# Kernel optimization log

Measured on AMD Instinct MI355X. Metric: run time of the kernel, lower is better.

Reference implementation:

```python
import jax, jax.numpy as jnp
import numpy as np

N_NEURONS = 256
P_MAX = 8
N_BLOCKS = P_MAX + 1
HIDDEN = 32
BATCH = 8192


def setup_inputs() -> dict:
    key = jax.random.key(0)
    ks = jax.random.split(key, 9)
    z = jax.random.normal(ks[0], (BATCH, N_BLOCKS * N_NEURONS), dtype=jnp.float32)
    # Per-block ScalarMLP params, stacked over the n_blocks axis.
    s1 = 1.0 / np.sqrt(N_NEURONS)
    s2 = 1.0 / np.sqrt(HIDDEN)
    gW1 = jax.random.uniform(ks[1], (N_BLOCKS, N_NEURONS, HIDDEN), jnp.float32, -s1, s1)
    gb1 = jax.random.uniform(ks[2], (N_BLOCKS, HIDDEN), jnp.float32, -s1, s1)
    gW2 = jax.random.uniform(ks[3], (N_BLOCKS, HIDDEN, HIDDEN), jnp.float32, -s2, s2)
    gb2 = jax.random.uniform(ks[4], (N_BLOCKS, HIDDEN), jnp.float32, -s2, s2)
    gW3 = jax.random.uniform(ks[5], (N_BLOCKS, HIDDEN), jnp.float32, -s2, s2)
    gb3 = jax.random.uniform(ks[6], (N_BLOCKS,), jnp.float32, -s2, s2)
    # Lag coupling matrices W_r ~ U(-init_scale, init_scale), init_scale=0.1
    W = jax.random.uniform(ks[7], (P_MAX, N_NEURONS, N_NEURONS), jnp.float32, -0.1, 0.1)
    return {"z": z, "gW1": gW1, "gb1": gb1, "gW2": gW2, "gb2": gb2,
            "gW3": gW3, "gb3": gb3, "W": W}


def _energy(z, gW1, gb1, gW2, gb2, gW3, gb3, W):
    B = z.shape[0]
    blocks = z.reshape(B, N_BLOCKS, N_NEURONS)           # (B, K, n)
    # Per-block ScalarMLP energies (all blocks at once).
    h1 = jax.nn.silu(jnp.einsum('bkn,knh->bkh', blocks, gW1) + gb1)   # (B, K, H)
    h2 = jax.nn.silu(jnp.einsum('bkh,khg->bkg', h1, gW2) + gb2)       # (B, K, H)
    e = jnp.einsum('bkh,kh->bk', h2, gW3) + gb3                        # (B, K)
    # Bilinear lag couplings: z_future^T W_r z_{lag-r}, r = 1..p_max.
    z_future = blocks[:, P_MAX, :]                                     # (B, n)
    lags = blocks[:, :P_MAX, :][:, ::-1, :]                            # (B, p, n), index r-1 == block p_max-r
    cross = jnp.einsum('bi,rij,brj->b', z_future, W, lags)             # (B,)
    return e.sum(axis=-1) + cross                                      # (B,)


def reference(z, gW1, gb1, gW2, gb2, gW3, gb3, W):
    # Score s(z) = -grad_z U(z); sum over batch gives per-sample grads
    # since energies are independent across samples.
    grad_z = jax.grad(lambda zz: _energy(zz, gW1, gb1, gW2, gb2, gW3, gb3, W).sum())(z)
    return -grad_z
```

## Files before the change

### kernel.cpp

```cpp
#include <hip/hip_runtime.h>
#include <hip/hip_bf16.h>
#include <math.h>

#define BATCH 8192
#define NB 9
#define NN 256
#define PMAX 8
#define HID 32
#define ZDIM 2304

typedef short bf16x8 __attribute__((ext_vector_type(8)));
typedef float f32x4 __attribute__((ext_vector_type(4)));

static __device__ inline unsigned short f2bf(float f) {
    __hip_bfloat16 h = __float2bfloat16(f);
    return *reinterpret_cast<unsigned short*>(&h);
}

static __device__ inline uint4 pack8(float4 a, float4 b) {
    uint4 u;
    u.x = (unsigned)f2bf(a.x) | ((unsigned)f2bf(a.y) << 16);
    u.y = (unsigned)f2bf(a.z) | ((unsigned)f2bf(a.w) << 16);
    u.z = (unsigned)f2bf(b.x) | ((unsigned)f2bf(b.y) << 16);
    u.w = (unsigned)f2bf(b.z) | ((unsigned)f2bf(b.w) << 16);
    return u;
}

__global__ __launch_bounds__(256) void k_pack(
    const float* __restrict__ W, const float* __restrict__ gW1,
    unsigned short* __restrict__ Wb, unsigned short* __restrict__ WTb,
    unsigned short* __restrict__ gW1b, unsigned short* __restrict__ g1Tb) {
    int r = blockIdx.z;
    int t = threadIdx.x;
    if (r < 8) {
        __shared__ float tt[32][33];
        int i0 = blockIdx.y * 32;
        int j0 = blockIdx.x * 32;
        int tx = t & 31;
        int ty = t >> 5;
        const float* src = W + (size_t)r * 65536;
        #pragma unroll
        for (int s = 0; s < 32; s += 8) {
            float v = src[(size_t)(i0 + ty + s) * 256 + (j0 + tx)];
            tt[ty + s][tx] = v;
            Wb[(size_t)r * 65536 + (size_t)(i0 + ty + s) * 256 + (j0 + tx)] = f2bf(v);
        }
        __syncthreads();
        #pragma unroll
        for (int s = 0; s < 32; s += 8)
            WTb[(size_t)r * 65536 + (size_t)(j0 + ty + s) * 256 + (i0 + tx)] = f2bf(tt[tx][ty + s]);
    } else {
        int tg = (blockIdx.y * 8 + blockIdx.x) * 256 + t;
        for (int e = tg; e < 73728; e += 16384) {
            float v = gW1[e];
            unsigned short b = f2bf(v);
            gW1b[e] = b;
            int k = e >> 13, n = (e >> 5) & 255, h = e & 31;
            g1Tb[(size_t)(k * 32 + h) * 256 + n] = b;
        }
    }
}

__global__ __launch_bounds__(256) void k_mlp(
    const float* __restrict__ z, const unsigned short* __restrict__ g1Tb,
    const float* __restrict__ gb1, const float* __restrict__ gW2,
    const float* __restrict__ gb2, const float* __restrict__ gW3,
    float* __restrict__ d1ws) {
    __shared__ uint4 As4[2][512];
    __shared__ uint4 Bw[1024];
    __shared__ uint4 W2Ts4[128];
    __shared__ uint4 W2Ns4[128];

    int t = threadIdx.x;
    int lane = t & 63;
    int w = t >> 6;
    int k = blockIdx.y;
    int b0 = blockIdx.x * 128;

    const unsigned short* bsrc = g1Tb + (size_t)k * 8192;
    for (int e = t; e < 1024; e += 256) {
        int h = e >> 5;
        int rest = e & 31;
        int c = rest >> 2, qq = rest & 3;
        Bw[c * 128 + (h & 15) + 16 * qq + 64 * (h >> 4)] =
            *(const uint4*)(bsrc + (size_t)h * 256 + c * 32 + qq * 8);
    }
    const float* gw2 = gW2 + (size_t)k * 1024;
    unsigned short* w2t = (unsigned short*)W2Ts4;
    unsigned short* w2n = (unsigned short*)W2Ns4;
    for (int e = t; e < 1024; e += 256) {
        int n = e >> 5, kk = e & 31;
        int qq = kk >> 3, jj = kk & 7;
        int ci = (n & 15) + 16 * qq + 64 * (n >> 4);
        w2t[ci * 8 + jj] = f2bf(gw2[kk * 32 + n]);
        w2n[ci * 8 + jj] = f2bf(gw2[n * 32 + kk]);
    }

    int mq = t >> 2;
    int q = t & 3;
    int ci0 = (mq & 15) + 16 * q + 64 * (mq >> 4);

    f32x4 acc1[2][2];
    #pragma unroll
    for (int i = 0; i < 2; ++i)
        #pragma unroll
        for (int j = 0; j < 2; ++j) acc1[i][j] = (f32x4){0.f, 0.f, 0.f, 0.f};

    auto loadZ = [&](int c, float4 (&fa)[2][2]) {
        #pragma unroll
        for (int pp = 0; pp < 2; ++pp) {
            int m = mq + 64 * pp;
            const float* as = z + (size_t)(b0 + m) * ZDIM + k * 256 + c * 32 + q * 8;
            fa[pp][0] = *(const float4*)(as);
            fa[pp][1] = *(const float4*)(as + 4);
        }
    };
    auto storeA = [&](int buf, float4 (&fa)[2][2]) {
        #pragma unroll
        for (int pp = 0; pp < 2; ++pp)
            As4[buf][ci0 + 256 * pp] = pack8(fa[pp][0], fa[pp][1]);
    };

    {
        float4 fa[2][2];
        loadZ(0, fa);
        storeA(0, fa);
    }
    int cur = 0;
    for (int c = 0; c < 8; ++c) {
        __syncthreads();
        float4 fan[2][2];
        if (c < 7) loadZ(c + 1, fan);
        bf16x8 af[2], bfr[2];
        #pragma unroll
        for (int i = 0; i < 2; ++i) af[i] = __builtin_bit_cast(bf16x8, As4[cur][lane + (w * 2 + i) * 64]);
        #pragma unroll
        for (int j = 0; j < 2; ++j) bfr[j] = __builtin_bit_cast(bf16x8, Bw[c * 128 + lane + j * 64]);
        #pragma unroll
        for (int i = 0; i < 2; ++i)
            #pragma unroll
            for (int j = 0; j < 2; ++j)
                acc1[i][j] = __builtin_amdgcn_mfma_f32_16x16x32_bf16(af[i], bfr[j], acc1[i][j], 0, 0, 0);
        if (c < 7) storeA(cur ^ 1, fan);
        cur ^= 1;
    }

    int cq = lane >> 4;
    int ci16 = lane & 15;
    float b1v[2], b2v[2], g3v[2];
    #pragma unroll
    for (int j = 0; j < 2; ++j) {
        b1v[j] = gb1[k * 32 + j * 16 + ci16];
        b2v[j] = gb2[k * 32 + j * 16 + ci16];
        g3v[j] = gW3[k * 32 + j * 16 + ci16];
    }
    unsigned short* Hs = (unsigned short*)As4;
    float sp1[2][2][4];
    __syncthreads();
    #pragma unroll
    for (int i = 0; i < 2; ++i)
        #pragma unroll
        for (int j = 0; j < 2; ++j)
            #pragma unroll
            for (int r = 0; r < 4; ++r) {
                float a1 = acc1[i][j][r] + b1v[j];
                float s1 = 1.f / (1.f + __expf(-a1));
                sp1[i][j][r] = s1 * (1.f + a1 * (1.f - s1));
                int row = w * 32 + i * 16 + cq * 4 + r;
                int col = j * 16 + ci16;
                int chunk = (row & 15) + 16 * (col >> 3) + 64 * (row >> 4);
                Hs[chunk * 8 + (col & 7)] = f2bf(a1 * s1);
            }
    __syncthreads();

    bf16x8 af2[2], wf[2];
    #pragma unroll
    for (int i = 0; i < 2; ++i) af2[i] = __builtin_bit_cast(bf16x8, As4[0][lane + (w * 2 + i) * 64]);
    #pragma unroll
    for (int j = 0; j < 2; ++j) wf[j] = __builtin_bit_cast(bf16x8, W2Ts4[lane + j * 64]);
    f32x4 acc2[2][2];
    #pragma unroll
    for (int i = 0; i < 2; ++i)
        #pragma unroll
        for (int j = 0; j < 2; ++j) {
            acc2[i][j] = (f32x4){0.f, 0.f, 0.f, 0.f};
            acc2[i][j] = __builtin_amdgcn_mfma_f32_16x16x32_bf16(af2[i], wf[j], acc2[i][j], 0, 0, 0);
        }

    __syncthreads();
    #pragma unroll
    for (int i = 0; i < 2; ++i)
        #pragma unroll
        for (int j = 0; j < 2; ++j)
            #pragma unroll
            for (int r = 0; r < 4; ++r) {
                float a2 = acc2[i][j][r] + b2v[j];
                float s2 = 1.f / (1.f + __expf(-a2));
                float da2 = g3v[j] * s2 * (1.f + a2 * (1.f - s2));
                int row = w * 32 + i * 16 + cq * 4 + r;
                int col = j * 16 + ci16;
                int chunk = (row & 15) + 16 * (col >> 3) + 64 * (row >> 4);
                Hs[chunk * 8 + (col & 7)] = f2bf(da2);
            }
    __syncthreads();

    bf16x8 af3[2], wg[2];
    #pragma unroll
    for (int i = 0; i < 2; ++i) af3[i] = __builtin_bit_cast(bf16x8, As4[0][lane + (w * 2 + i) * 64]);
    #pragma unroll
    for (int j = 0; j < 2; ++j) wg[j] = __builtin_bit_cast(bf16x8, W2Ns4[lane + j * 64]);
    #pragma unroll
    for (int i = 0; i < 2; ++i)
        #pragma unroll
        for (int j = 0; j < 2; ++j) {
            f32x4 a3 = (f32x4){0.f, 0.f, 0.f, 0.f};
            a3 = __builtin_amdgcn_mfma_f32_16x16x32_bf16(af3[i], wg[j], a3, 0, 0, 0);
            #pragma unroll
            for (int r = 0; r < 4; ++r) {
                int row = w * 32 + i * 16 + cq * 4 + r;
                int col = j * 16 + ci16;
                d1ws[((size_t)k * BATCH + b0 + row) * 32 + col] = a3[r] * sp1[i][j][r];
            }
        }
}

__global__ __launch_bounds__(256) void k_gemm_lo(
    const float* __restrict__ z, const float* __restrict__ d1,
    const unsigned short* __restrict__ WTb, const unsigned short* __restrict__ gW1b,
    float* __restrict__ out) {
    __shared__ uint4 As4[2][512];
    __shared__ uint4 Bs4[2][512];

    int t = threadIdx.x;
    int lane = t & 63;
    int w = t >> 6;
    int wr = w >> 1, wc = w & 1;
    int b0 = blockIdx.x * 128;
    int n0 = blockIdx.y * 128;
    int k  = n0 >> 8;
    int jb = n0 & 255;

    const float* Amain = z + (size_t)b0 * ZDIM + 2048;
    const float* Aext  = d1 + ((size_t)k * BATCH + b0) * 32;
    const unsigned short* Bmain = WTb + (size_t)(7 - k) * 65536 + (size_t)jb * 256;
    const unsigned short* Bext  = gW1b + ((size_t)k * 256 + jb) * 32;

    int mq = t >> 2;
    int q  = t & 3;
    int ci0 = (mq & 15) + 16 * q + 64 * (mq >> 4);

    auto loadAB = [&](int c, float4 (&fa)[2][2], uint4 (&bu)[2]) {
        #pragma unroll
        for (int pp = 0; pp < 2; ++pp) {
            int m = mq + 64 * pp;
            const float* as = (c < 8) ? (Amain + (size_t)m * ZDIM + c * 32 + q * 8)
                                      : (Aext + (size_t)m * 32 + q * 8);
            fa[pp][0] = *(const float4*)(as);
            fa[pp][1] = *(const float4*)(as + 4);
            const unsigned short* bs = (c < 8) ? (Bmain + (size_t)m * 256 + c * 32 + q * 8)
                                               : (Bext + (size_t)m * 32 + q * 8);
            bu[pp] = *(const uint4*)(bs);
        }
    };
    auto storeAB = [&](int buf, float4 (&fa)[2][2], uint4 (&bu)[2]) {
        #pragma unroll
        for (int pp = 0; pp < 2; ++pp) {
            int idx = ci0 + 256 * pp;
            As4[buf][idx] = pack8(fa[pp][0], fa[pp][1]);
            Bs4[buf][idx] = bu[pp];
        }
    };

    f32x4 acc[4][4];
    #pragma unroll
    for (int i = 0; i < 4; ++i)
        #pragma unroll
        for (int j = 0; j < 4; ++j) acc[i][j] = (f32x4){0.f, 0.f, 0.f, 0.f};

    {
        float4 fa[2][2]; uint4 bu[2];
        loadAB(0, fa, bu);
        storeAB(0, fa, bu);
    }
    int cur = 0;
    for (int c = 0; c < 9; ++c) {
        __syncthreads();
        float4 fan[2][2]; uint4 bun[2];
        if (c < 8) loadAB(c + 1, fan, bun);
        bf16x8 af[4], bf[4];
        #pragma unroll
        for (int i = 0; i < 4; ++i) af[i] = __builtin_bit_cast(bf16x8, As4[cur][lane + (wr * 4 + i) * 64]);
        #pragma unroll
        for (int j = 0; j < 4; ++j) bf[j] = __builtin_bit_cast(bf16x8, Bs4[cur][lane + (wc * 4 + j) * 64]);
        #pragma unroll
        for (int i = 0; i < 4; ++i)
            #pragma unroll
            for (int j = 0; j < 4; ++j)
                acc[i][j] = __builtin_amdgcn_mfma_f32_16x16x32_bf16(af[i], bf[j], acc[i][j], 0, 0, 0);
        if (c < 8) storeAB(cur ^ 1, fan, bun);
        cur ^= 1;
    }

    int rquad = lane >> 4;
    int cidx  = lane & 15;
    #pragma unroll
    for (int i = 0; i < 4; ++i) {
        #pragma unroll
        for (int j = 0; j < 4; ++j) {
            float* o = out + (size_t)(b0 + wr * 64 + i * 16 + rquad * 4) * ZDIM
                     + (k * 256 + jb + wc * 64 + j * 16 + cidx);
            #pragma unroll
            for (int r = 0; r < 4; ++r)
                o[(size_t)r * ZDIM] = -acc[i][j][r];
        }
    }
}

__global__ __launch_bounds__(256) void k_gemm_hi(
    const float* __restrict__ z, const float* __restrict__ d1,
    const unsigned short* __restrict__ Wb, const unsigned short* __restrict__ gW1b,
    float* __restrict__ out) {
    __shared__ uint4 As4[2][512];
    __shared__ uint4 Bs4[2][512];

    int t = threadIdx.x;
    int lane = t & 63;
    int w = t >> 6;
    int wr = w & 1, wc = w >> 1;
    int b0 = blockIdx.x * 64;
    int i0 = blockIdx.y * 64;

    const float* Amain = z + (size_t)b0 * ZDIM;
    const float* Aext  = d1 + ((size_t)8 * BATCH + b0) * 32;
    const unsigned short* Bext = gW1b + (size_t)(8 * 256 + i0) * 32;

    int m = t >> 2;
    int q = t & 3;
    int ci = (m & 15) + 16 * q + 64 * (m >> 4);

    auto loadAB = [&](int c, float4 (&fa)[2][2], uint4 (&bu)[2]) {
        if (c < 32) {
            int kb = c * 64;
            #pragma unroll
            for (int h = 0; h < 2; ++h) {
                const float* as = Amain + (size_t)m * ZDIM + kb + h * 32 + q * 8;
                fa[h][0] = *(const float4*)(as);
                fa[h][1] = *(const float4*)(as + 4);
            }
            int lag = kb >> 8;
            int j0  = kb & 255;
            const unsigned short* bs = Wb + (size_t)(7 - lag) * 65536
                                         + (size_t)(i0 + m) * 256 + j0 + q * 8;
            bu[0] = *(const uint4*)(bs);
            bu[1] = *(const uint4*)(bs + 32);
        } else {
            const float* as = Aext + (size_t)m * 32 + q * 8;
            fa[0][0] = *(const float4*)(as);
            fa[0][1] = *(const float4*)(as + 4);
            fa[1][0] = make_float4(0.f, 0.f, 0.f, 0.f);
            fa[1][1] = make_float4(0.f, 0.f, 0.f, 0.f);
            bu[0] = *(const uint4*)(Bext + (size_t)m * 32 + q * 8);
            bu[1] = make_uint4(0u, 0u, 0u, 0u);
        }
    };
    auto storeAB = [&](int buf, float4 (&fa)[2][2], uint4 (&bu)[2]) {
        #pragma unroll
        for (int h = 0; h < 2; ++h) {
            As4[buf][h * 256 + ci] = pack8(fa[h][0], fa[h][1]);
            Bs4[buf][h * 256 + ci] = bu[h];
        }
    };

    f32x4 acc[2][2];
    #pragma unroll
    for (int i = 0; i < 2; ++i)
        #pragma unroll
        for (int j = 0; j < 2; ++j) acc[i][j] = (f32x4){0.f, 0.f, 0.f, 0.f};

    {
        float4 fa[2][2]; uint4 bu[2];
        loadAB(0, fa, bu);
        storeAB(0, fa, bu);
    }
    int cur = 0;
    for (int c = 0; c < 33; ++c) {
        __syncthreads();
        float4 fan[2][2]; uint4 bun[2];
        if (c < 32) loadAB(c + 1, fan, bun);
        #pragma unroll
        for (int h = 0; h < 2; ++h) {
            bf16x8 af[2], bf[2];
            #pragma unroll
            for (int i = 0; i < 2; ++i)
                af[i] = __builtin_bit_cast(bf16x8, As4[cur][h * 256 + lane + (wr * 2 + i) * 64]);
            #pragma unroll
            for (int j = 0; j < 2; ++j)
                bf[j] = __builtin_bit_cast(bf16x8, Bs4[cur][h * 256 + lane + (wc * 2 + j) * 64]);
            #pragma unroll
            for (int i = 0; i < 2; ++i)
                #pragma unroll
                for (int j = 0; j < 2; ++j)
                    acc[i][j] = __builtin_amdgcn_mfma_f32_16x16x32_bf16(af[i], bf[j], acc[i][j], 0, 0, 0);
        }
        if (c < 32) storeAB(cur ^ 1, fan, bun);
        cur ^= 1;
    }

    int rquad = lane >> 4;
    int cidx  = lane & 15;
    #pragma unroll
    for (int i = 0; i < 2; ++i) {
        #pragma unroll
        for (int j = 0; j < 2; ++j) {
            float* o = out + (size_t)(b0 + wr * 32 + i * 16 + rquad * 4) * ZDIM
                     + (2048 + i0 + wc * 32 + j * 16 + cidx);
            #pragma unroll
            for (int r = 0; r < 4; ++r)
                o[(size_t)r * ZDIM] = -acc[i][j][r];
        }
    }
}

extern "C" void kernel_launch(void* const* d_in, const int* in_sizes, int n_in,
                              void* d_out, int out_size, void* d_ws, size_t ws_size,
                              hipStream_t stream) {
    const float* z   = (const float*)d_in[0];
    const float* gW1 = (const float*)d_in[1];
    const float* gb1 = (const float*)d_in[2];
    const float* gW2 = (const float*)d_in[3];
    const float* gb2 = (const float*)d_in[4];
    const float* gW3 = (const float*)d_in[5];
    const float* W   = (const float*)d_in[7];
    float* out = (float*)d_out;

    float* ws = (float*)d_ws;
    float*          d1ws = ws;
    unsigned short* Wb   = (unsigned short*)(ws + 2359296);
    unsigned short* WTb  = Wb + 524288;
    unsigned short* gW1b = WTb + 524288;
    unsigned short* g1Tb = gW1b + 73728;

    k_pack<<<dim3(8, 8, 9), 256, 0, stream>>>(W, gW1, Wb, WTb, gW1b, g1Tb);
    k_mlp<<<dim3(64, 9), 256, 0, stream>>>(z, g1Tb, gb1, gW2, gb2, gW3, d1ws);
    k_gemm_lo<<<dim3(64, 16), 256, 0, stream>>>(z, d1ws, WTb, gW1b, out);
    k_gemm_hi<<<dim3(128, 4), 256, 0, stream>>>(z, d1ws, Wb, gW1b, out);
}
```

Before: 199.8 us.

## Cache bf16 z from MLP kernel and merge both gradient GEMMs into one launch

The MLP kernel now writes its bf16-packed copy of z to a workspace buffer as it streams z. The two gradient GEMM kernels are merged into a single launch that branches on block index, and both halves read bf16 z instead of fp32 z, which halves their A-operand traffic and drops the repeated conversion. This adds an extra bf16 write of z (about 37 MB) in the MLP kernel. In exchange it removes a launch and lets the lo and hi GEMM blocks run concurrently.

Result: slower. 206.6 us (+3.4%).

```diff
diff --git a/kernel.cpp b/kernel.cpp
--- a/kernel.cpp
+++ b/kernel.cpp
@@ -65,7 +65,7 @@
     const float* __restrict__ z, const unsigned short* __restrict__ g1Tb,
     const float* __restrict__ gb1, const float* __restrict__ gW2,
     const float* __restrict__ gb2, const float* __restrict__ gW3,
-    float* __restrict__ d1ws) {
+    float* __restrict__ d1ws, unsigned short* __restrict__ zb) {
     __shared__ uint4 As4[2][512];
     __shared__ uint4 Bw[1024];
     __shared__ uint4 W2Ts4[128];
@@ -115,16 +115,20 @@
             fa[pp][1] = *(const float4*)(as + 4);
         }
     };
-    auto storeA = [&](int buf, float4 (&fa)[2][2]) {
-        #pragma unroll
-        for (int pp = 0; pp < 2; ++pp)
-            As4[buf][ci0 + 256 * pp] = pack8(fa[pp][0], fa[pp][1]);
+    auto sinkZ = [&](int buf, int c, float4 (&fa)[2][2]) {
+        #pragma unroll
+        for (int pp = 0; pp < 2; ++pp) {
+            uint4 pk = pack8(fa[pp][0], fa[pp][1]);
+            As4[buf][ci0 + 256 * pp] = pk;
+            int m = mq + 64 * pp;
+            *(uint4*)(zb + (size_t)(b0 + m) * ZDIM + k * 256 + c * 32 + q * 8) = pk;
+        }
     };
 
     {
         float4 fa[2][2];
         loadZ(0, fa);
-        storeA(0, fa);
+        sinkZ(0, 0, fa);
     }
     int cur = 0;
     for (int c = 0; c < 8; ++c) {
@@ -141,7 +145,7 @@
             #pragma unroll
             for (int j = 0; j < 2; ++j)
                 acc1[i][j] = __builtin_amdgcn_mfma_f32_16x16x32_bf16(af[i], bfr[j], acc1[i][j], 0, 0, 0);
-        if (c < 7) storeA(cur ^ 1, fan);
+        if (c < 7) sinkZ(cur ^ 1, c + 1, fan);
         cur ^= 1;
     }
 
@@ -224,199 +228,189 @@
         }
 }
 
-__global__ __launch_bounds__(256) void k_gemm_lo(
-    const float* __restrict__ z, const float* __restrict__ d1,
-    const unsigned short* __restrict__ WTb, const unsigned short* __restrict__ gW1b,
-    float* __restrict__ out) {
+__global__ __launch_bounds__(256) void k_gemm(
+    const unsigned short* __restrict__ zb, const float* __restrict__ d1,
+    const unsigned short* __restrict__ Wb, const unsigned short* __restrict__ WTb,
+    const unsigned short* __restrict__ gW1b, float* __restrict__ out) {
     __shared__ uint4 As4[2][512];
     __shared__ uint4 Bs4[2][512];
 
+    int id = blockIdx.x;
     int t = threadIdx.x;
     int lane = t & 63;
     int w = t >> 6;
-    int wr = w >> 1, wc = w & 1;
-    int b0 = blockIdx.x * 128;
-    int n0 = blockIdx.y * 128;
-    int k  = n0 >> 8;
-    int jb = n0 & 255;
-
-    const float* Amain = z + (size_t)b0 * ZDIM + 2048;
-    const float* Aext  = d1 + ((size_t)k * BATCH + b0) * 32;
-    const unsigned short* Bmain = WTb + (size_t)(7 - k) * 65536 + (size_t)jb * 256;
-    const unsigned short* Bext  = gW1b + ((size_t)k * 256 + jb) * 32;
-
-    int mq = t >> 2;
-    int q  = t & 3;
-    int ci0 = (mq & 15) + 16 * q + 64 * (mq >> 4);
-
-    auto loadAB = [&](int c, float4 (&fa)[2][2], uint4 (&bu)[2]) {
-        #pragma unroll
-        for (int pp = 0; pp < 2; ++pp) {
-            int m = mq + 64 * pp;
-            const float* as = (c < 8) ? (Amain + (size_t)m * ZDIM + c * 32 + q * 8)
-                                      : (Aext + (size_t)m * 32 + q * 8);
-            fa[pp][0] = *(const float4*)(as);
-            fa[pp][1] = *(const float4*)(as + 4);
-            const unsigned short* bs = (c < 8) ? (Bmain + (size_t)m * 256 + c * 32 + q * 8)
-                                               : (Bext + (size_t)m * 32 + q * 8);
-            bu[pp] = *(const uint4*)(bs);
-        }
-    };
-    auto storeAB = [&](int buf, float4 (&fa)[2][2], uint4 (&bu)[2]) {
-        #pragma unroll
-        for (int pp = 0; pp < 2; ++pp) {
-            int idx = ci0 + 256 * pp;
-            As4[buf][idx] = pack8(fa[pp][0], fa[pp][1]);
-            Bs4[buf][idx] = bu[pp];
-        }
-    };
-
-    f32x4 acc[4][4];
-    #pragma unroll
-    for (int i = 0; i < 4; ++i)
-        #pragma unroll
-        for (int j = 0; j < 4; ++j) acc[i][j] = (f32x4){0.f, 0.f, 0.f, 0.f};
-
-    {
-        float4 fa[2][2]; uint4 bu[2];
-        loadAB(0, fa, bu);
-        storeAB(0, fa, bu);
-    }
-    int cur = 0;
-    for (int c = 0; c < 9; ++c) {
-        __syncthreads();
-        float4 fan[2][2]; uint4 bun[2];
-        if (c < 8) loadAB(c + 1, fan, bun);
-        bf16x8 af[4], bf[4];
-        #pragma unroll
-        for (int i = 0; i < 4; ++i) af[i] = __builtin_bit_cast(bf16x8, As4[cur][lane + (wr * 4 + i) * 64]);
-        #pragma unroll
-        for (int j = 0; j < 4; ++j) bf[j] = __builtin_bit_cast(bf16x8, Bs4[cur][lane + (wc * 4 + j) * 64]);
+
+    if (id < 1024) {
+        int wr = w >> 1, wc = w & 1;
+        int b0 = (id & 63) * 128;
+        int n0 = (id >> 6) * 128;
+        int k  = n0 >> 8;
+        int jb = n0 & 255;
+
+        const unsigned short* Azb = zb + (size_t)b0 * ZDIM + 2048;
+        const float* Aext  = d1 + ((size_t)k * BATCH + b0) * 32;
+        const unsigned short* Bmain = WTb + (size_t)(7 - k) * 65536 + (size_t)jb * 256;
+        const unsigned short* Bext  = gW1b + ((size_t)k * 256 + jb) * 32;
+
+        int mq = t >> 2;
+        int q  = t & 3;
+        int ci0 = (mq & 15) + 16 * q + 64 * (mq >> 4);
+
+        auto loadAB = [&](int c, uint4 (&au)[2], uint4 (&bu)[2]) {
+            #pragma unroll
+            for (int pp = 0; pp < 2; ++pp) {
+                int m = mq + 64 * pp;
+                if (c < 8) {
+                    au[pp] = *(const uint4*)(Azb + (size_t)m * ZDIM + c * 32 + q * 8);
+                    bu[pp] = *(const uint4*)(Bmain + (size_t)m * 256 + c * 32 + q * 8);
+                } else {
+                    const float* as = Aext + (size_t)m * 32 + q * 8;
+                    au[pp] = pack8(*(const float4*)(as), *(const float4*)(as + 4));
+                    bu[pp] = *(const uint4*)(Bext + (size_t)m * 32 + q * 8);
+                }
+            }
+        };
+        auto storeAB = [&](int buf, uint4 (&au)[2], uint4 (&bu)[2]) {
+            #pragma unroll
+            for (int pp = 0; pp < 2; ++pp) {
+                int idx = ci0 + 256 * pp;
+                As4[buf][idx] = au[pp];
+                Bs4[buf][idx] = bu[pp];
+            }
+        };
+
+        f32x4 acc[4][4];
         #pragma unroll
         for (int i = 0; i < 4; ++i)
             #pragma unroll
-            for (int j = 0; j < 4; ++j)
-                acc[i][j] = __builtin_amdgcn_mfma_f32_16x16x32_bf16(af[i], bf[j], acc[i][j], 0, 0, 0);
-        if (c < 8) storeAB(cur ^ 1, fan, bun);
-        cur ^= 1;
-    }
-
-    int rquad = lane >> 4;
-    int cidx  = lane & 15;
-    #pragma unroll
-    for (int i = 0; i < 4; ++i) {
-        #pragma unroll
-        for (int j = 0; j < 4; ++j) {
-            float* o = out + (size_t)(b0 + wr * 64 + i * 16 + rquad * 4) * ZDIM
-                     + (k * 256 + jb + wc * 64 + j * 16 + cidx);
-            #pragma unroll
-            for (int r = 0; r < 4; ++r)
-                o[(size_t)r * ZDIM] = -acc[i][j][r];
-        }
-    }
-}
-
-__global__ __launch_bounds__(256) void k_gemm_hi(
-    const float* __restrict__ z, const float* __restrict__ d1,
-    const unsigned short* __restrict__ Wb, const unsigned short* __restrict__ gW1b,
-    float* __restrict__ out) {
-    __shared__ uint4 As4[2][512];
-    __shared__ uint4 Bs4[2][512];
-
-    int t = threadIdx.x;
-    int lane = t & 63;
-    int w = t >> 6;
-    int wr = w & 1, wc = w >> 1;
-    int b0 = blockIdx.x * 64;
-    int i0 = blockIdx.y * 64;
-
-    const float* Amain = z + (size_t)b0 * ZDIM;
-    const float* Aext  = d1 + ((size_t)8 * BATCH + b0) * 32;
-    const unsigned short* Bext = gW1b + (size_t)(8 * 256 + i0) * 32;
-
-    int m = t >> 2;
-    int q = t & 3;
-    int ci = (m & 15) + 16 * q + 64 * (m >> 4);
-
-    auto loadAB = [&](int c, float4 (&fa)[2][2], uint4 (&bu)[2]) {
-        if (c < 32) {
-            int kb = c * 64;
+            for (int j = 0; j < 4; ++j) acc[i][j] = (f32x4){0.f, 0.f, 0.f, 0.f};
+
+        {
+            uint4 au[2], bu[2];
+            loadAB(0, au, bu);
+            storeAB(0, au, bu);
+        }
+        int cur = 0;
+        for (int c = 0; c < 9; ++c) {
+            __syncthreads();
+            uint4 aun[2], bun[2];
+            if (c < 8) loadAB(c + 1, aun, bun);
+            bf16x8 af[4], bf[4];
+            #pragma unroll
+            for (int i = 0; i < 4; ++i) af[i] = __builtin_bit_cast(bf16x8, As4[cur][lane + (wr * 4 + i) * 64]);
+            #pragma unroll
+            for (int j = 0; j < 4; ++j) bf[j] = __builtin_bit_cast(bf16x8, Bs4[cur][lane + (wc * 4 + j) * 64]);
+            #pragma unroll
+            for (int i = 0; i < 4; ++i)
+                #pragma unroll
+                for (int j = 0; j < 4; ++j)
+                    acc[i][j] = __builtin_amdgcn_mfma_f32_16x16x32_bf16(af[i], bf[j], acc[i][j], 0, 0, 0);
+            if (c < 8) storeAB(cur ^ 1, aun, bun);
+            cur ^= 1;
+        }
+
+        int rquad = lane >> 4;
+        int cidx  = lane & 15;
+        #pragma unroll
+        for (int i = 0; i < 4; ++i) {
+            #pragma unroll
+            for (int j = 0; j < 4; ++j) {
+                float* o = out + (size_t)(b0 + wr * 64 + i * 16 + rquad * 4) * ZDIM
+                         + (k * 256 + jb + wc * 64 + j * 16 + cidx);
+                #pragma unroll
+                for (int r = 0; r < 4; ++r)
+                    o[(size_t)r * ZDIM] = -acc[i][j][r];
+            }
+        }
+    } else {
+        int id2 = id - 1024;
+        int wr = w & 1, wc = w >> 1;
+        int b0 = (id2 & 127) * 64;
+        int i0 = (id2 >> 7) * 64;
+
+        const unsigned short* Azb = zb + (size_t)b0 * ZDIM;
+        const float* Aext  = d1 + ((size_t)8 * BATCH + b0) * 32;
+        const unsigned short* Bext = gW1b + (size_t)(8 * 256 + i0) * 32;
+
+        int m = t >> 2;
+        int q = t & 3;
+        int ci = (m & 15) + 16 * q + 64 * (m >> 4);
+
+        auto loadAB = [&](int c, uint4 (&au)[2], uint4 (&bu)[2]) {
+            if (c < 32) {
+                int kb = c * 64;
+                #pragma unroll
+                for (int h = 0; h < 2; ++h)
+                    au[h] = *(const uint4*)(Azb + (size_t)m * ZDIM + kb + h * 32 + q * 8);
+                int lag = kb >> 8;
+                int j0  = kb & 255;
+                const unsigned short* bs = Wb + (size_t)(7 - lag) * 65536
+                                             + (size_t)(i0 + m) * 256 + j0 + q * 8;
+                bu[0] = *(const uint4*)(bs);
+                bu[1] = *(const uint4*)(bs + 32);
+            } else {
+                const float* as = Aext + (size_t)m * 32 + q * 8;
+                au[0] = pack8(*(const float4*)(as), *(const float4*)(as + 4));
+                au[1] = make_uint4(0u, 0u, 0u, 0u);
+                bu[0] = *(const uint4*)(Bext + (size_t)m * 32 + q * 8);
+                bu[1] = make_uint4(0u, 0u, 0u, 0u);
+            }
+        };
+        auto storeAB = [&](int buf, uint4 (&au)[2], uint4 (&bu)[2]) {
             #pragma unroll
             for (int h = 0; h < 2; ++h) {
-                const float* as = Amain + (size_t)m * ZDIM + kb + h * 32 + q * 8;
-                fa[h][0] = *(const float4*)(as);
-                fa[h][1] = *(const float4*)(as + 4);
-            }
-            int lag = kb >> 8;
-            int j0  = kb & 255;
-            const unsigned short* bs = Wb + (size_t)(7 - lag) * 65536
-                                         + (size_t)(i0 + m) * 256 + j0 + q * 8;
-            bu[0] = *(const uint4*)(bs);
-            bu[1] = *(const uint4*)(bs + 32);
-        } else {
-            const float* as = Aext + (size_t)m * 32 + q * 8;
-            fa[0][0] = *(const float4*)(as);
-            fa[0][1] = *(const float4*)(as + 4);
-            fa[1][0] = make_float4(0.f, 0.f, 0.f, 0.f);
-            fa[1][1] = make_float4(0.f, 0.f, 0.f, 0.f);
-            bu[0] = *(const uint4*)(Bext + (size_t)m * 32 + q * 8);
-            bu[1] = make_uint4(0u, 0u, 0u, 0u);
-        }
-    };
-    auto storeAB = [&](int buf, float4 (&fa)[2][2], uint4 (&bu)[2]) {
-        #pragma unroll
-        for (int h = 0; h < 2; ++h) {
-            As4[buf][h * 256 + ci] = pack8(fa[h][0], fa[h][1]);
-            Bs4[buf][h * 256 + ci] = bu[h];
-        }
-    };
-
-    f32x4 acc[2][2];
-    #pragma unroll
-    for (int i = 0; i < 2; ++i)
-        #pragma unroll
-        for (int j = 0; j < 2; ++j) acc[i][j] = (f32x4){0.f, 0.f, 0.f, 0.f};
-
-    {
-        float4 fa[2][2]; uint4 bu[2];
-        loadAB(0, fa, bu);
-        storeAB(0, fa, bu);
-    }
-    int cur = 0;
-    for (int c = 0; c < 33; ++c) {
-        __syncthreads();
-        float4 fan[2][2]; uint4 bun[2];
-        if (c < 32) loadAB(c + 1, fan, bun);
-        #pragma unroll
-        for (int h = 0; h < 2; ++h) {
-            bf16x8 af[2], bf[2];
-            #pragma unroll
-            for (int i = 0; i < 2; ++i)
-                af[i] = __builtin_bit_cast(bf16x8, As4[cur][h * 256 + lane + (wr * 2 + i) * 64]);
-            #pragma unroll
-            for (int j = 0; j < 2; ++j)
-                bf[j] = __builtin_bit_cast(bf16x8, Bs4[cur][h * 256 + lane + (wc * 2 + j) * 64]);
-            #pragma unroll
-            for (int i = 0; i < 2; ++i)
+                As4[buf][h * 256 + ci] = au[h];
+                Bs4[buf][h * 256 + ci] = bu[h];
+            }
+        };
+
+        f32x4 acc[2][2];
+        #pragma unroll
+        for (int i = 0; i < 2; ++i)
+            #pragma unroll
+            for (int j = 0; j < 2; ++j) acc[i][j] = (f32x4){0.f, 0.f, 0.f, 0.f};
+
+        {
+            uint4 au[2], bu[2];
+            loadAB(0, au, bu);
+            storeAB(0, au, bu);
+        }
+        int cur = 0;
+        for (int c = 0; c < 33; ++c) {
+            __syncthreads();
+            uint4 aun[2], bun[2];
+            if (c < 32) loadAB(c + 1, aun, bun);
+            #pragma unroll
+            for (int h = 0; h < 2; ++h) {
+                bf16x8 af[2], bf[2];
+                #pragma unroll
+                for (int i = 0; i < 2; ++i)
+                    af[i] = __builtin_bit_cast(bf16x8, As4[cur][h * 256 + lane + (wr * 2 + i) * 64]);
                 #pragma unroll
                 for (int j = 0; j < 2; ++j)
-                    acc[i][j] = __builtin_amdgcn_mfma_f32_16x16x32_bf16(af[i], bf[j], acc[i][j], 0, 0, 0);
-        }
-        if (c < 32) storeAB(cur ^ 1, fan, bun);
-        cur ^= 1;
-    }
-
-    int rquad = lane >> 4;
-    int cidx  = lane & 15;
-    #pragma unroll
-    for (int i = 0; i < 2; ++i) {
-        #pragma unroll
-        for (int j = 0; j < 2; ++j) {
-            float* o = out + (size_t)(b0 + wr * 32 + i * 16 + rquad * 4) * ZDIM
-                     + (2048 + i0 + wc * 32 + j * 16 + cidx);
-            #pragma unroll
-            for (int r = 0; r < 4; ++r)
-                o[(size_t)r * ZDIM] = -acc[i][j][r];
+                    bf[j] = __builtin_bit_cast(bf16x8, Bs4[cur][h * 256 + lane + (wc * 2 + j) * 64]);
+                #pragma unroll
+                for (int i = 0; i < 2; ++i)
+                    #pragma unroll
+                    for (int j = 0; j < 2; ++j)
+                        acc[i][j] = __builtin_amdgcn_mfma_f32_16x16x32_bf16(af[i], bf[j], acc[i][j], 0, 0, 0);
+            }
+            if (c < 32) storeAB(cur ^ 1, aun, bun);
+            cur ^= 1;
+        }
+
+        int rquad = lane >> 4;
+        int cidx  = lane & 15;
+        #pragma unroll
+        for (int i = 0; i < 2; ++i) {
+            #pragma unroll
+            for (int j = 0; j < 2; ++j) {
+                float* o = out + (size_t)(b0 + wr * 32 + i * 16 + rquad * 4) * ZDIM
+                         + (2048 + i0 + wc * 32 + j * 16 + cidx);
+                #pragma unroll
+                for (int r = 0; r < 4; ++r)
+                    o[(size_t)r * ZDIM] = -acc[i][j][r];
+            }
         }
     }
 }
@@ -439,9 +433,9 @@
     unsigned short* WTb  = Wb + 524288;
     unsigned short* gW1b = WTb + 524288;
     unsigned short* g1Tb = gW1b + 73728;
+    unsigned short* zb   = g1Tb + 73728;
 
     k_pack<<<dim3(8, 8, 9), 256, 0, stream>>>(W, gW1, Wb, WTb, gW1b, g1Tb);
-    k_mlp<<<dim3(64, 9), 256, 0, stream>>>(z, g1Tb, gb1, gW2, gb2, gW3, d1ws);
-    k_gemm_lo<<<dim3(64, 16), 256, 0, stream>>>(z, d1ws, WTb, gW1b, out);
-    k_gemm_hi<<<dim3(128, 4), 256, 0, stream>>>(z, d1ws, Wb, gW1b, out);
-}
+    k_mlp<<<dim3(64, 9), 256, 0, stream>>>(z, g1Tb, gb1, gW2, gb2, gW3, d1ws, zb);
+    k_gemm<<<dim3(1536), 256, 0, stream>>>(zb, d1ws, Wb, WTb, gW1b, out);
+}
```

## Split k_gemm_hi reduction dimension across two 256-thread halves with LDS reduction

Applied to the files above, without the earlier changes.

k_gemm_hi now launches 512 threads per block, and the two halves each take half of the K=2048 lag dimension (4 lags each). Half 0 also handles the extra gW1 chunk. Each iteration processes a 32-wide K slice instead of 64, and partial accumulators are combined through shared memory before the store. This doubles in-block parallelism on the long serial K loop of a small-grid kernel, at the cost of more barriers per unit of work and a reduction step.

Result: slower. 206.7 us (+3.4%).

```diff
diff --git a/kernel.cpp b/kernel.cpp
--- a/kernel.cpp
+++ b/kernel.cpp
@@ -316,59 +316,52 @@
     }
 }
 
-__global__ __launch_bounds__(256) void k_gemm_hi(
+__global__ __launch_bounds__(512) void k_gemm_hi(
     const float* __restrict__ z, const float* __restrict__ d1,
     const unsigned short* __restrict__ Wb, const unsigned short* __restrict__ gW1b,
     float* __restrict__ out) {
-    __shared__ uint4 As4[2][512];
-    __shared__ uint4 Bs4[2][512];
+    __shared__ uint4 As4[2][2][256];
+    __shared__ uint4 Bs4[2][2][256];
 
     int t = threadIdx.x;
+    int half = t >> 8;
+    int tt = t & 255;
     int lane = t & 63;
-    int w = t >> 6;
+    int w = (tt >> 6);
     int wr = w & 1, wc = w >> 1;
     int b0 = blockIdx.x * 64;
     int i0 = blockIdx.y * 64;
 
-    const float* Amain = z + (size_t)b0 * ZDIM;
+    const float* Amain = z + (size_t)b0 * ZDIM + half * 1024;
     const float* Aext  = d1 + ((size_t)8 * BATCH + b0) * 32;
     const unsigned short* Bext = gW1b + (size_t)(8 * 256 + i0) * 32;
 
-    int m = t >> 2;
-    int q = t & 3;
+    int m = tt >> 2;
+    int q = tt & 3;
     int ci = (m & 15) + 16 * q + 64 * (m >> 4);
 
-    auto loadAB = [&](int c, float4 (&fa)[2][2], uint4 (&bu)[2]) {
+    int nc = (half == 0) ? 33 : 32;
+
+    auto loadAB = [&](int c, float4 (&fa)[2], uint4& bu) {
         if (c < 32) {
-            int kb = c * 64;
-            #pragma unroll
-            for (int h = 0; h < 2; ++h) {
-                const float* as = Amain + (size_t)m * ZDIM + kb + h * 32 + q * 8;
-                fa[h][0] = *(const float4*)(as);
-                fa[h][1] = *(const float4*)(as + 4);
-            }
-            int lag = kb >> 8;
+            int kb = c * 32;
+            const float* as = Amain + (size_t)m * ZDIM + kb + q * 8;
+            fa[0] = *(const float4*)(as);
+            fa[1] = *(const float4*)(as + 4);
+            int lag = half * 4 + (c >> 3);
             int j0  = kb & 255;
-            const unsigned short* bs = Wb + (size_t)(7 - lag) * 65536
-                                         + (size_t)(i0 + m) * 256 + j0 + q * 8;
-            bu[0] = *(const uint4*)(bs);
-            bu[1] = *(const uint4*)(bs + 32);
+            bu = *(const uint4*)(Wb + (size_t)(7 - lag) * 65536
+                                    + (size_t)(i0 + m) * 256 + j0 + q * 8);
         } else {
             const float* as = Aext + (size_t)m * 32 + q * 8;
-            fa[0][0] = *(const float4*)(as);
-            fa[0][1] = *(const float4*)(as + 4);
-            fa[1][0] = make_float4(0.f, 0.f, 0.f, 0.f);
-            fa[1][1] = make_float4(0.f, 0.f, 0.f, 0.f);
-            bu[0] = *(const uint4*)(Bext + (size_t)m * 32 + q * 8);
-            bu[1] = make_uint4(0u, 0u, 0u, 0u);
-        }
-    };
-    auto storeAB = [&](int buf, float4 (&fa)[2][2], uint4 (&bu)[2]) {
-        #pragma unroll
-        for (int h = 0; h < 2; ++h) {
-            As4[buf][h * 256 + ci] = pack8(fa[h][0], fa[h][1]);
-            Bs4[buf][h * 256 + ci] = bu[h];
-        }
+            fa[0] = *(const float4*)(as);
+            fa[1] = *(const float4*)(as + 4);
+            bu = *(const uint4*)(Bext + (size_t)m * 32 + q * 8);
+        }
+    };
+    auto storeAB = [&](int buf, float4 (&fa)[2], uint4& bu) {
+        As4[half][buf][ci] = pack8(fa[0], fa[1]);
+        Bs4[half][buf][ci] = bu;
     };
 
     f32x4 acc[2][2];
@@ -378,45 +371,62 @@
         for (int j = 0; j < 2; ++j) acc[i][j] = (f32x4){0.f, 0.f, 0.f, 0.f};
 
     {
-        float4 fa[2][2]; uint4 bu[2];
+        float4 fa[2]; uint4 bu;
         loadAB(0, fa, bu);
         storeAB(0, fa, bu);
     }
     int cur = 0;
     for (int c = 0; c < 33; ++c) {
         __syncthreads();
-        float4 fan[2][2]; uint4 bun[2];
-        if (c < 32) loadAB(c + 1, fan, bun);
-        #pragma unroll
-        for (int h = 0; h < 2; ++h) {
+        float4 fan[2]; uint4 bun;
+        bool ldn = (c + 1 < nc);
+        if (ldn) loadAB(c + 1, fan, bun);
+        if (c < nc) {
             bf16x8 af[2], bf[2];
             #pragma unroll
             for (int i = 0; i < 2; ++i)
-                af[i] = __builtin_bit_cast(bf16x8, As4[cur][h * 256 + lane + (wr * 2 + i) * 64]);
+                af[i] = __builtin_bit_cast(bf16x8, As4[half][cur][lane + (wr * 2 + i) * 64]);
             #pragma unroll
             for (int j = 0; j < 2; ++j)
-                bf[j] = __builtin_bit_cast(bf16x8, Bs4[cur][h * 256 + lane + (wc * 2 + j) * 64]);
+                bf[j] = __builtin_bit_cast(bf16x8, Bs4[half][cur][lane + (wc * 2 + j) * 64]);
             #pragma unroll
             for (int i = 0; i < 2; ++i)
                 #pragma unroll
                 for (int j = 0; j < 2; ++j)
                     acc[i][j] = __builtin_amdgcn_mfma_f32_16x16x32_bf16(af[i], bf[j], acc[i][j], 0, 0, 0);
         }
-        if (c < 32) storeAB(cur ^ 1, fan, bun);
+        if (ldn) storeAB(cur ^ 1, fan, bun);
         cur ^= 1;
     }
 
+    __syncthreads();
+    float* red = (float*)(&As4[0][0][0]);
     int rquad = lane >> 4;
     int cidx  = lane & 15;
-    #pragma unroll
-    for (int i = 0; i < 2; ++i) {
-        #pragma unroll
-        for (int j = 0; j < 2; ++j) {
-            float* o = out + (size_t)(b0 + wr * 32 + i * 16 + rquad * 4) * ZDIM
-                     + (2048 + i0 + wc * 32 + j * 16 + cidx);
-            #pragma unroll
-            for (int r = 0; r < 4; ++r)
-                o[(size_t)r * ZDIM] = -acc[i][j][r];
+    if (half == 1) {
+        #pragma unroll
+        for (int i = 0; i < 2; ++i)
+            #pragma unroll
+            for (int j = 0; j < 2; ++j)
+                #pragma unroll
+                for (int r = 0; r < 4; ++r)
+                    red[(wr * 32 + i * 16 + rquad * 4 + r) * 64
+                        + (wc * 32 + j * 16 + cidx)] = acc[i][j][r];
+    }
+    __syncthreads();
+    if (half == 0) {
+        #pragma unroll
+        for (int i = 0; i < 2; ++i) {
+            #pragma unroll
+            for (int j = 0; j < 2; ++j) {
+                #pragma unroll
+                for (int r = 0; r < 4; ++r) {
+                    int lr = wr * 32 + i * 16 + rquad * 4 + r;
+                    int lc = wc * 32 + j * 16 + cidx;
+                    float v = acc[i][j][r] + red[lr * 64 + lc];
+                    out[(size_t)(b0 + lr) * ZDIM + 2048 + i0 + lc] = -v;
+                }
+            }
         }
     }
 }
@@ -443,5 +453,5 @@
     k_pack<<<dim3(8, 8, 9), 256, 0, stream>>>(W, gW1, Wb, WTb, gW1b, g1Tb);
     k_mlp<<<dim3(64, 9), 256, 0, stream>>>(z, g1Tb, gb1, gW2, gb2, gW3, d1ws);
     k_gemm_lo<<<dim3(64, 16), 256, 0, stream>>>(z, d1ws, WTb, gW1b, out);
-    k_gemm_hi<<<dim3(128, 4), 256, 0, stream>>>(z, d1ws, Wb, gW1b, out);
-}
+    k_gemm_hi<<<dim3(128, 4), 512, 0, stream>>>(z, d1ws, Wb, gW1b, out);
+}
```

## Merge lo and hi GEMM kernels into one interleaved launch

Applied to the files above, without the earlier changes.

Combines the two output GEMM kernels into a single 1536-block launch. Block indices are interleaved so that every third block runs the hi (lag-coupling) tile and the other two run lo tiles. This removes one kernel launch and the serialization between the two GEMMs, letting the short lo tiles and the long hi tiles share the GPU at the same time. Register usage is now set by whichever branch needs more, which may lower occupancy for the other branch.

Result: slower. 212.2 us (+6.2%).

```diff
diff --git a/kernel.cpp b/kernel.cpp
--- a/kernel.cpp
+++ b/kernel.cpp
@@ -224,199 +224,196 @@
         }
 }
 
-__global__ __launch_bounds__(256) void k_gemm_lo(
+__global__ __launch_bounds__(256) void k_gemm(
     const float* __restrict__ z, const float* __restrict__ d1,
-    const unsigned short* __restrict__ WTb, const unsigned short* __restrict__ gW1b,
-    float* __restrict__ out) {
+    const unsigned short* __restrict__ Wb, const unsigned short* __restrict__ WTb,
+    const unsigned short* __restrict__ gW1b, float* __restrict__ out) {
     __shared__ uint4 As4[2][512];
     __shared__ uint4 Bs4[2][512];
 
+    int g = blockIdx.x;
     int t = threadIdx.x;
     int lane = t & 63;
     int w = t >> 6;
-    int wr = w >> 1, wc = w & 1;
-    int b0 = blockIdx.x * 128;
-    int n0 = blockIdx.y * 128;
-    int k  = n0 >> 8;
-    int jb = n0 & 255;
-
-    const float* Amain = z + (size_t)b0 * ZDIM + 2048;
-    const float* Aext  = d1 + ((size_t)k * BATCH + b0) * 32;
-    const unsigned short* Bmain = WTb + (size_t)(7 - k) * 65536 + (size_t)jb * 256;
-    const unsigned short* Bext  = gW1b + ((size_t)k * 256 + jb) * 32;
-
-    int mq = t >> 2;
-    int q  = t & 3;
-    int ci0 = (mq & 15) + 16 * q + 64 * (mq >> 4);
-
-    auto loadAB = [&](int c, float4 (&fa)[2][2], uint4 (&bu)[2]) {
-        #pragma unroll
-        for (int pp = 0; pp < 2; ++pp) {
-            int m = mq + 64 * pp;
-            const float* as = (c < 8) ? (Amain + (size_t)m * ZDIM + c * 32 + q * 8)
-                                      : (Aext + (size_t)m * 32 + q * 8);
-            fa[pp][0] = *(const float4*)(as);
-            fa[pp][1] = *(const float4*)(as + 4);
-            const unsigned short* bs = (c < 8) ? (Bmain + (size_t)m * 256 + c * 32 + q * 8)
-                                               : (Bext + (size_t)m * 32 + q * 8);
-            bu[pp] = *(const uint4*)(bs);
-        }
-    };
-    auto storeAB = [&](int buf, float4 (&fa)[2][2], uint4 (&bu)[2]) {
-        #pragma unroll
-        for (int pp = 0; pp < 2; ++pp) {
-            int idx = ci0 + 256 * pp;
-            As4[buf][idx] = pack8(fa[pp][0], fa[pp][1]);
-            Bs4[buf][idx] = bu[pp];
-        }
-    };
-
-    f32x4 acc[4][4];
-    #pragma unroll
-    for (int i = 0; i < 4; ++i)
-        #pragma unroll
-        for (int j = 0; j < 4; ++j) acc[i][j] = (f32x4){0.f, 0.f, 0.f, 0.f};
-
-    {
-        float4 fa[2][2]; uint4 bu[2];
-        loadAB(0, fa, bu);
-        storeAB(0, fa, bu);
-    }
-    int cur = 0;
-    for (int c = 0; c < 9; ++c) {
-        __syncthreads();
-        float4 fan[2][2]; uint4 bun[2];
-        if (c < 8) loadAB(c + 1, fan, bun);
-        bf16x8 af[4], bf[4];
-        #pragma unroll
-        for (int i = 0; i < 4; ++i) af[i] = __builtin_bit_cast(bf16x8, As4[cur][lane + (wr * 4 + i) * 64]);
-        #pragma unroll
-        for (int j = 0; j < 4; ++j) bf[j] = __builtin_bit_cast(bf16x8, Bs4[cur][lane + (wc * 4 + j) * 64]);
+    int rr = g % 3;
+    int q3 = g / 3;
+
+    if (rr != 0) {
+        int lo_n = q3 * 2 + (rr - 1);
+        int wr = w >> 1, wc = w & 1;
+        int b0 = (lo_n & 63) * 128;
+        int n0 = (lo_n >> 6) * 128;
+        int k  = n0 >> 8;
+        int jb = n0 & 255;
+
+        const float* Amain = z + (size_t)b0 * ZDIM + 2048;
+        const float* Aext  = d1 + ((size_t)k * BATCH + b0) * 32;
+        const unsigned short* Bmain = WTb + (size_t)(7 - k) * 65536 + (size_t)jb * 256;
+        const unsigned short* Bext  = gW1b + ((size_t)k * 256 + jb) * 32;
+
+        int mq = t >> 2;
+        int q  = t & 3;
+        int ci0 = (mq & 15) + 16 * q + 64 * (mq >> 4);
+
+        auto loadAB = [&](int c, float4 (&fa)[2][2], uint4 (&bu)[2]) {
+            #pragma unroll
+            for (int pp = 0; pp < 2; ++pp) {
+                int m = mq + 64 * pp;
+                const float* as = (c < 8) ? (Amain + (size_t)m * ZDIM + c * 32 + q * 8)
+                                          : (Aext + (size_t)m * 32 + q * 8);
+                fa[pp][0] = *(const float4*)(as);
+                fa[pp][1] = *(const float4*)(as + 4);
+                const unsigned short* bs = (c < 8) ? (Bmain + (size_t)m * 256 + c * 32 + q * 8)
+                                                   : (Bext + (size_t)m * 32 + q * 8);
+                bu[pp] = *(const uint4*)(bs);
+            }
+        };
+        auto storeAB = [&](int buf, float4 (&fa)[2][2], uint4 (&bu)[2]) {
+            #pragma unroll
+            for (int pp = 0; pp < 2; ++pp) {
+                int idx = ci0 + 256 * pp;
+                As4[buf][idx] = pack8(fa[pp][0], fa[pp][1]);
+                Bs4[buf][idx] = bu[pp];
+            }
+        };
+
+        f32x4 acc[4][4];
         #pragma unroll
         for (int i = 0; i < 4; ++i)
             #pragma unroll
-            for (int j = 0; j < 4; ++j)
-                acc[i][j] = __builtin_amdgcn_mfma_f32_16x16x32_bf16(af[i], bf[j], acc[i][j], 0, 0, 0);
-        if (c < 8) storeAB(cur ^ 1, fan, bun);
-        cur ^= 1;
-    }
-
-    int rquad = lane >> 4;
-    int cidx  = lane & 15;
-    #pragma unroll
-    for (int i = 0; i < 4; ++i) {
-        #pragma unroll
-        for (int j = 0; j < 4; ++j) {
-            float* o = out + (size_t)(b0 + wr * 64 + i * 16 + rquad * 4) * ZDIM
-                     + (k * 256 + jb + wc * 64 + j * 16 + cidx);
-            #pragma unroll
-            for (int r = 0; r < 4; ++r)
-                o[(size_t)r * ZDIM] = -acc[i][j][r];
-        }
-    }
-}
-
-__global__ __launch_bounds__(256) void k_gemm_hi(
-    const float* __restrict__ z, const float* __restrict__ d1,
-    const unsigned short* __restrict__ Wb, const unsigned short* __restrict__ gW1b,
-    float* __restrict__ out) {
-    __shared__ uint4 As4[2][512];
-    __shared__ uint4 Bs4[2][512];
-
-    int t = threadIdx.x;
-    int lane = t & 63;
-    int w = t >> 6;
-    int wr = w & 1, wc = w >> 1;
-    int b0 = blockIdx.x * 64;
-    int i0 = blockIdx.y * 64;
-
-    const float* Amain = z + (size_t)b0 * ZDIM;
-    const float* Aext  = d1 + ((size_t)8 * BATCH + b0) * 32;
-    const unsigned short* Bext = gW1b + (size_t)(8 * 256 + i0) * 32;
-
-    int m = t >> 2;
-    int q = t & 3;
-    int ci = (m & 15) + 16 * q + 64 * (m >> 4);
-
-    auto loadAB = [&](int c, float4 (&fa)[2][2], uint4 (&bu)[2]) {
-        if (c < 32) {
-            int kb = c * 64;
+            for (int j = 0; j < 4; ++j) acc[i][j] = (f32x4){0.f, 0.f, 0.f, 0.f};
+
+        {
+            float4 fa[2][2]; uint4 bu[2];
+            loadAB(0, fa, bu);
+            storeAB(0, fa, bu);
+        }
+        int cur = 0;
+        for (int c = 0; c < 9; ++c) {
+            __syncthreads();
+            float4 fan[2][2]; uint4 bun[2];
+            if (c < 8) loadAB(c + 1, fan, bun);
+            bf16x8 af[4], bf[4];
+            #pragma unroll
+            for (int i = 0; i < 4; ++i) af[i] = __builtin_bit_cast(bf16x8, As4[cur][lane + (wr * 4 + i) * 64]);
+            #pragma unroll
+            for (int j = 0; j < 4; ++j) bf[j] = __builtin_bit_cast(bf16x8, Bs4[cur][lane + (wc * 4 + j) * 64]);
+            #pragma unroll
+            for (int i = 0; i < 4; ++i)
+                #pragma unroll
+                for (int j = 0; j < 4; ++j)
+                    acc[i][j] = __builtin_amdgcn_mfma_f32_16x16x32_bf16(af[i], bf[j], acc[i][j], 0, 0, 0);
+            if (c < 8) storeAB(cur ^ 1, fan, bun);
+            cur ^= 1;
+        }
+
+        int rquad = lane >> 4;
+        int cidx  = lane & 15;
+        #pragma unroll
+        for (int i = 0; i < 4; ++i) {
+            #pragma unroll
+            for (int j = 0; j < 4; ++j) {
+                float* o = out + (size_t)(b0 + wr * 64 + i * 16 + rquad * 4) * ZDIM
+                         + (k * 256 + jb + wc * 64 + j * 16 + cidx);
+                #pragma unroll
+                for (int r = 0; r < 4; ++r)
+                    o[(size_t)r * ZDIM] = -acc[i][j][r];
+            }
+        }
+    } else {
+        int hi_n = q3;
+        int wr = w & 1, wc = w >> 1;
+        int b0 = (hi_n & 127) * 64;
+        int i0 = (hi_n >> 7) * 64;
+
+        const float* Amain = z + (size_t)b0 * ZDIM;
+        const float* Aext  = d1 + ((size_t)8 * BATCH + b0) * 32;
+        const unsigned short* Bext = gW1b + (size_t)(8 * 256 + i0) * 32;
+
+        int m = t >> 2;
+        int q = t & 3;
+        int ci = (m & 15) + 16 * q + 64 * (m >> 4);
+
+        auto loadAB = [&](int c, float4 (&fa)[2][2], uint4 (&bu)[2]) {
+            if (c < 32) {
+                int kb = c * 64;
+                #pragma unroll
+                for (int h = 0; h < 2; ++h) {
+                    const float* as = Amain + (size_t)m * ZDIM + kb + h * 32 + q * 8;
+                    fa[h][0] = *(const float4*)(as);
+                    fa[h][1] = *(const float4*)(as + 4);
+                }
+                int lag = kb >> 8;
+                int j0  = kb & 255;
+                const unsigned short* bs = Wb + (size_t)(7 - lag) * 65536
+                                             + (size_t)(i0 + m) * 256 + j0 + q * 8;
+                bu[0] = *(const uint4*)(bs);
+                bu[1] = *(const uint4*)(bs + 32);
+            } else {
+                const float* as = Aext + (size_t)m * 32 + q * 8;
+                fa[0][0] = *(const float4*)(as);
+                fa[0][1] = *(const float4*)(as + 4);
+                fa[1][0] = make_float4(0.f, 0.f, 0.f, 0.f);
+                fa[1][1] = make_float4(0.f, 0.f, 0.f, 0.f);
+                bu[0] = *(const uint4*)(Bext + (size_t)m * 32 + q * 8);
+                bu[1] = make_uint4(0u, 0u, 0u, 0u);
+            }
+        };
+        auto storeAB = [&](int buf, float4 (&fa)[2][2], uint4 (&bu)[2]) {
             #pragma unroll
             for (int h = 0; h < 2; ++h) {
-                const float* as = Amain + (size_t)m * ZDIM + kb + h * 32 + q * 8;
-                fa[h][0] = *(const float4*)(as);
-                fa[h][1] = *(const float4*)(as + 4);
-            }
-            int lag = kb >> 8;
-            int j0  = kb & 255;
-            const unsigned short* bs = Wb + (size_t)(7 - lag) * 65536
-                                         + (size_t)(i0 + m) * 256 + j0 + q * 8;
-            bu[0] = *(const uint4*)(bs);
-            bu[1] = *(const uint4*)(bs + 32);
-        } else {
-            const float* as = Aext + (size_t)m * 32 + q * 8;
-            fa[0][0] = *(const float4*)(as);
-            fa[0][1] = *(const float4*)(as + 4);
-            fa[1][0] = make_float4(0.f, 0.f, 0.f, 0.f);
-            fa[1][1] = make_float4(0.f, 0.f, 0.f, 0.f);
-            bu[0] = *(const uint4*)(Bext + (size_t)m * 32 + q * 8);
-            bu[1] = make_uint4(0u, 0u, 0u, 0u);
-        }
-    };
-    auto storeAB = [&](int buf, float4 (&fa)[2][2], uint4 (&bu)[2]) {
-        #pragma unroll
-        for (int h = 0; h < 2; ++h) {
-            As4[buf][h * 256 + ci] = pack8(fa[h][0], fa[h][1]);
-            Bs4[buf][h * 256 + ci] = bu[h];
-        }
-    };
-
-    f32x4 acc[2][2];
-    #pragma unroll
-    for (int i = 0; i < 2; ++i)
-        #pragma unroll
-        for (int j = 0; j < 2; ++j) acc[i][j] = (f32x4){0.f, 0.f, 0.f, 0.f};
-
-    {
-        float4 fa[2][2]; uint4 bu[2];
-        loadAB(0, fa, bu);
-        storeAB(0, fa, bu);
-    }
-    int cur = 0;
-    for (int c = 0; c < 33; ++c) {
-        __syncthreads();
-        float4 fan[2][2]; uint4 bun[2];
-        if (c < 32) loadAB(c + 1, fan, bun);
-        #pragma unroll
-        for (int h = 0; h < 2; ++h) {
-            bf16x8 af[2], bf[2];
-            #pragma unroll
-            for (int i = 0; i < 2; ++i)
-                af[i] = __builtin_bit_cast(bf16x8, As4[cur][h * 256 + lane + (wr * 2 + i) * 64]);
-            #pragma unroll
-            for (int j = 0; j < 2; ++j)
-                bf[j] = __builtin_bit_cast(bf16x8, Bs4[cur][h * 256 + lane + (wc * 2 + j) * 64]);
-            #pragma unroll
-            for (int i = 0; i < 2; ++i)
+                As4[buf][h * 256 + ci] = pack8(fa[h][0], fa[h][1]);
+                Bs4[buf][h * 256 + ci] = bu[h];
+            }
+        };
+
+        f32x4 acc[2][2];
+        #pragma unroll
+        for (int i = 0; i < 2; ++i)
+            #pragma unroll
+            for (int j = 0; j < 2; ++j) acc[i][j] = (f32x4){0.f, 0.f, 0.f, 0.f};
+
+        {
+            float4 fa[2][2]; uint4 bu[2];
+            loadAB(0, fa, bu);
+            storeAB(0, fa, bu);
+        }
+        int cur = 0;
+        for (int c = 0; c < 33; ++c) {
+            __syncthreads();
+            float4 fan[2][2]; uint4 bun[2];
+            if (c < 32) loadAB(c + 1, fan, bun);
+            #pragma unroll
+            for (int h = 0; h < 2; ++h) {
+                bf16x8 af[2], bf[2];
+                #pragma unroll
+                for (int i = 0; i < 2; ++i)
+                    af[i] = __builtin_bit_cast(bf16x8, As4[cur][h * 256 + lane + (wr * 2 + i) * 64]);
                 #pragma unroll
                 for (int j = 0; j < 2; ++j)
-                    acc[i][j] = __builtin_amdgcn_mfma_f32_16x16x32_bf16(af[i], bf[j], acc[i][j], 0, 0, 0);
-        }
-        if (c < 32) storeAB(cur ^ 1, fan, bun);
-        cur ^= 1;
-    }
-
-    int rquad = lane >> 4;
-    int cidx  = lane & 15;
-    #pragma unroll
-    for (int i = 0; i < 2; ++i) {
-        #pragma unroll
-        for (int j = 0; j < 2; ++j) {
-            float* o = out + (size_t)(b0 + wr * 32 + i * 16 + rquad * 4) * ZDIM
-                     + (2048 + i0 + wc * 32 + j * 16 + cidx);
-            #pragma unroll
-            for (int r = 0; r < 4; ++r)
-                o[(size_t)r * ZDIM] = -acc[i][j][r];
+                    bf[j] = __builtin_bit_cast(bf16x8, Bs4[cur][h * 256 + lane + (wc * 2 + j) * 64]);
+                #pragma unroll
+                for (int i = 0; i < 2; ++i)
+                    #pragma unroll
+                    for (int j = 0; j < 2; ++j)
+                        acc[i][j] = __builtin_amdgcn_mfma_f32_16x16x32_bf16(af[i], bf[j], acc[i][j], 0, 0, 0);
+            }
+            if (c < 32) storeAB(cur ^ 1, fan, bun);
+            cur ^= 1;
+        }
+
+        int rquad = lane >> 4;
+        int cidx  = lane & 15;
+        #pragma unroll
+        for (int i = 0; i < 2; ++i) {
+            #pragma unroll
+            for (int j = 0; j < 2; ++j) {
+                float* o = out + (size_t)(b0 + wr * 32 + i * 16 + rquad * 4) * ZDIM
+                         + (2048 + i0 + wc * 32 + j * 16 + cidx);
+                #pragma unroll
+                for (int r = 0; r < 4; ++r)
+                    o[(size_t)r * ZDIM] = -acc[i][j][r];
+            }
         }
     }
 }
@@ -442,6 +439,5 @@
 
     k_pack<<<dim3(8, 8, 9), 256, 0, stream>>>(W, gW1, Wb, WTb, gW1b, g1Tb);
     k_mlp<<<dim3(64, 9), 256, 0, stream>>>(z, g1Tb, gb1, gW2, gb2, gW3, d1ws);
-    k_gemm_lo<<<dim3(64, 16), 256, 0, stream>>>(z, d1ws, WTb, gW1b, out);
-    k_gemm_hi<<<dim3(128, 4), 256, 0, stream>>>(z, d1ws, Wb, gW1b, out);
-}
+    k_gemm<<<dim3(1536), 256, 0, stream>>>(z, d1ws, Wb, WTb, gW1b, out);
+}
```
